# Kernel optimization log

Measured on AMD Instinct MI355X. Metric: run time of the kernel, lower is better.

## Reference

```python
import jax, jax.numpy as jnp
import numpy as np

N_NODES = 100000
N_EDGES = 3200000
N_GRAPHS = 4096
IN_DIM = 128
HID = 64
EPS = 1e-5


def setup_inputs() -> dict:
    key = jax.random.key(0)
    ks = jax.random.split(key, 16)
    x = jax.random.normal(ks[0], (N_NODES, IN_DIM), dtype=jnp.float32)
    edge_index = jax.random.randint(ks[1], (2, N_EDGES), 0, N_NODES, dtype=jnp.int32)
    batch = jnp.sort(jax.random.randint(ks[2], (N_NODES,), 0, N_GRAPHS, dtype=jnp.int32))

    def lin(k, fan_in, fan_out):
        s = 1.0 / np.sqrt(fan_in)
        kw, kb = jax.random.split(k)
        W = jax.random.uniform(kw, (fan_in, fan_out), minval=-s, maxval=s, dtype=jnp.float32)
        b = jax.random.uniform(kb, (fan_out,), minval=-s, maxval=s, dtype=jnp.float32)
        return W, b

    Wc0, bc0 = lin(ks[3], IN_DIM, HID)
    Wc1, bc1 = lin(ks[4], HID, HID)
    Wc2, bc2 = lin(ks[5], HID, HID)
    W1, b1 = lin(ks[6], HID, HID)
    W2, b2 = lin(ks[7], HID, 1)
    ones = jnp.ones((HID,), jnp.float32)
    zeros = jnp.zeros((HID,), jnp.float32)
    return {
        'x': x, 'edge_index': edge_index, 'batch': batch,
        'Wc0': Wc0, 'bc0': bc0, 'g0': ones, 'be0': zeros,
        'Wc1': Wc1, 'bc1': bc1, 'g1': ones, 'be1': zeros,
        'Wc2': Wc2, 'bc2': bc2, 'g2': ones, 'be2': zeros,
        'W1': W1, 'b1': b1, 'gf': ones, 'bf': zeros,
        'W2': W2, 'b2': b2,
    }


def _gcn_norm(edge_index):
    # Add self-loops, then symmetric normalization norm_e = d^-1/2[row] * d^-1/2[col]
    loops = jnp.arange(N_NODES, dtype=jnp.int32)
    row = jnp.concatenate([edge_index[0], loops])
    col = jnp.concatenate([edge_index[1], loops])
    deg = jax.ops.segment_sum(jnp.ones_like(col, jnp.float32), col, num_segments=N_NODES)
    dinv = jnp.where(deg > 0, jax.lax.rsqrt(deg), 0.0)
    norm = dinv[row] * dinv[col]
    return row, col, norm


def _gcn_conv(x, W, b, row, col, norm):
    h = x @ W                                   # [N, hid]
    msg = h[row] * norm[:, None]                # [E+N, hid] gather + scale
    out = jax.ops.segment_sum(msg, col, num_segments=N_NODES)  # scatter-add
    return out + b


def _bn(x, gamma, beta):
    mu = jnp.mean(x, axis=0)
    var = jnp.var(x, axis=0)
    return (x - mu) * jax.lax.rsqrt(var + EPS) * gamma + beta


def reference(x, edge_index, batch, Wc0, bc0, g0, be0, Wc1, bc1, g1, be1,
              Wc2, bc2, g2, be2, W1, b1, gf, bf, W2, b2):
    row, col, norm = _gcn_norm(edge_index)
    h = x
    for W, b, g, be in ((Wc0, bc0, g0, be0), (Wc1, bc1, g1, be1), (Wc2, bc2, g2, be2)):
        h = jax.nn.relu(_bn(_gcn_conv(h, W, b, row, col, norm), g, be))
    # global mean pool over graphs
    sums = jax.ops.segment_sum(h, batch, num_segments=N_GRAPHS)
    cnts = jax.ops.segment_sum(jnp.ones((N_NODES,), jnp.float32), batch, num_segments=N_GRAPHS)
    pooled = sums / jnp.maximum(cnts, 1.0)[:, None]  # [G, hid]
    z = jax.nn.relu(_bn(pooled @ W1 + b1, gf, bf))
    # dropout is identity at inference
    out = z @ W2 + b2
    return out.squeeze(-1)
```

## Files before the change

### kernel.cpp

```cpp
#include <hip/hip_runtime.h>
#include <hip/hip_bf16.h>

#define NN 100000
#define NE 3200000
#define NG 4096
#define NB 256
#define NBK 782

typedef unsigned short ushort_t;
typedef short short8 __attribute__((ext_vector_type(8)));
typedef float floatx4 __attribute__((ext_vector_type(4)));

__device__ __forceinline__ float bf2f(unsigned short u){
  union{unsigned int i; float f;} x; x.i = ((unsigned)u)<<16; return x.f;
}
__device__ __forceinline__ ushort_t f2bf(float f){
  union{float f; unsigned int i;} x; x.f = f;
  unsigned int r = x.i + 0x7fff + ((x.i >> 16) & 1);
  return (ushort_t)(r >> 16);
}


__global__ __launch_bounds__(512) void k_hist(const int* __restrict__ ei, int* __restrict__ histT){
  __shared__ int lh[NBK];
  int b = blockIdx.x, t = threadIdx.x;
  for (int k=t; k<NBK; k+=512) lh[k]=0;
  __syncthreads();
  int e0 = b*(NE/NB);
  for (int e=e0+t; e<e0+(NE/NB); e+=512) atomicAdd(&lh[ei[NE+e]>>7], 1);
  __syncthreads();
  for (int k=t; k<NBK; k+=512) histT[(size_t)k*NB+b] = lh[k];
}

__global__ __launch_bounds__(256) void k_scanA(int* __restrict__ histT, int* __restrict__ total){
  int wv = blockIdx.x*4 + (threadIdx.x>>6);
  int lane = threadIdx.x & 63;
  if (wv >= NBK) return;
  int* row = histT + (size_t)wv*NB;
  int carry = 0;
  #pragma unroll
  for (int ch=0; ch<NB/64; ++ch){
    int a = row[ch*64+lane];
    int inc = a;
    for (int off=1; off<64; off<<=1){
      int x = __shfl_up(inc, off, 64);
      if (lane >= off) inc += x;
    }
    row[ch*64+lane] = carry + inc - a;
    carry += __shfl(inc, 63, 64);
  }
  if (lane==0) total[wv] = carry;
}

__global__ void k_scanB(const int* __restrict__ total, int* __restrict__ base){
  __shared__ int lds[1024];
  int t = threadIdx.x;
  int v = (t < NBK)? total[t] : 0;
  lds[t] = v; __syncthreads();
  for (int off=1; off<1024; off<<=1){
    int x = (t>=off)? lds[t-off] : 0;
    __syncthreads();
    lds[t] += x;
    __syncthreads();
  }
  if (t < NBK)      base[t]   = lds[t]-v;
  if (t == NBK-1)   base[NBK] = lds[t];
}

__global__ __launch_bounds__(512) void k_pairs(const int* __restrict__ ei,
    const int* __restrict__ histT, const int* __restrict__ base,
    int* __restrict__ pairs){
  __shared__ int cur[NBK];
  int b = blockIdx.x, t = threadIdx.x;
  for (int k=t; k<NBK; k+=512) cur[k] = base[k] + histT[(size_t)k*NB + b];
  __syncthreads();
  int e0 = b*(NE/NB);
  for (int e=e0+t; e<e0+(NE/NB); e+=512){
    int src = ei[e], dst = ei[NE+e];
    int p = atomicAdd(&cur[dst>>7], 1);
    pairs[p] = (src << 7) | (dst & 127);
  }
}

__global__ __launch_bounds__(256) void k_fine(const int* __restrict__ pairs,
    const int* __restrict__ base, int* __restrict__ csr,
    int* __restrict__ colptr, float* __restrict__ dinv){
  __shared__ int cnt[128], off[128];
  int k = blockIdx.x, t = threadIdx.x;
  if (t < 128) cnt[t] = 0;
  __syncthreads();
  int s = base[k], e = base[k+1];
  for (int i=s+t; i<e; i+=256) atomicAdd(&cnt[pairs[i] & 127], 1);
  __syncthreads();
  int v = (t<128)? cnt[t] : 0;
  if (t<128) off[t] = v;
  __syncthreads();
  for (int o=1; o<128; o<<=1){
    int x = (t>=o && t<128)? off[t-o] : 0;
    __syncthreads();
    if (t<128) off[t] += x;
    __syncthreads();
  }
  int node0 = k*128;
  if (t < 128 && node0+t < NN){
    colptr[node0+t] = s + off[t] - v;
    dinv[node0+t]   = rsqrtf((float)cnt[t] + 1.0f);
  }
  if (k == NBK-1 && t == 0) colptr[NN] = NE;
  __syncthreads();
  if (t < 128) cnt[t] = off[t] - v;
  __syncthreads();
  for (int i=s+t; i<e; i+=256){
    int u = pairs[i];
    int p = s + atomicAdd(&cnt[u & 127], 1);
    csr[p] = u >> 7;
  }
}


__global__ __launch_bounds__(256) void k_gemm0m(const float* __restrict__ x,
    const float* __restrict__ W, const float* __restrict__ dinv,
    ushort_t* __restrict__ hs){
  __shared__ __attribute__((aligned(16))) ushort_t Wt[64*136];
  int t = threadIdx.x;
  for (int i=t; i<128*64; i+=256){
    int k = i>>6, n = i&63;
    Wt[n*136 + k] = f2bf(W[i]);
  }
  __syncthreads();
  int lane = t & 63, wv = t >> 6;
  int n0 = lane & 15, quad = lane >> 4;
  int r0 = blockIdx.x*64 + wv*16;
  int row = r0 + n0;
  int rowc = (row < NN)? row : NN-1;
  const float* xr = x + (size_t)rowc*128 + quad*8;
  floatx4 acc[4] = {{0,0,0,0},{0,0,0,0},{0,0,0,0},{0,0,0,0}};
  #pragma unroll
  for (int ks=0; ks<4; ++ks){
    float4 a01 = *(const float4*)(xr + ks*32);
    float4 a23 = *(const float4*)(xr + ks*32 + 4);
    short8 af;
    af[0]=(short)f2bf(a01.x); af[1]=(short)f2bf(a01.y);
    af[2]=(short)f2bf(a01.z); af[3]=(short)f2bf(a01.w);
    af[4]=(short)f2bf(a23.x); af[5]=(short)f2bf(a23.y);
    af[6]=(short)f2bf(a23.z); af[7]=(short)f2bf(a23.w);
    #pragma unroll
    for (int tl=0; tl<4; ++tl){
      short8 bf = *(const short8*)(&Wt[(tl*16+n0)*136 + ks*32 + quad*8]);
      acc[tl] = __builtin_amdgcn_mfma_f32_16x16x32_bf16(af, bf, acc[tl], 0, 0, 0);
    }
  }
  #pragma unroll
  for (int reg=0; reg<4; ++reg){
    int rr = r0 + quad*4 + reg;
    if (rr < NN){
      float dv = dinv[rr];
      #pragma unroll
      for (int tl=0; tl<4; ++tl)
        hs[(size_t)rr*64 + tl*16 + n0] = f2bf(acc[tl][reg]*dv);
    }
  }
}


__global__ __launch_bounds__(256) void k_gemmSm(const float* __restrict__ h,
    const float* __restrict__ W, const float* __restrict__ coeff,
    const float* __restrict__ dinv, ushort_t* __restrict__ hs){
  __shared__ __attribute__((aligned(16))) ushort_t Wt[64*72];
  int t = threadIdx.x;
  for (int i=t; i<64*64; i+=256){
    int k = i>>6, n = i&63;
    Wt[n*72 + k] = f2bf(W[i]);
  }
  __syncthreads();
  int lane = t & 63, wv = t >> 6;
  int n0 = lane & 15, quad = lane >> 4;
  int r0 = blockIdx.x*64 + wv*16;
  int row = r0 + n0;
  int rowc = (row < NN)? row : NN-1;
  const float* hr = h + (size_t)rowc*64 + quad*8;
  floatx4 acc[4] = {{0,0,0,0},{0,0,0,0},{0,0,0,0},{0,0,0,0}};
  #pragma unroll
  for (int ks=0; ks<2; ++ks){
    float4 a01 = *(const float4*)(hr + ks*32);
    float4 a23 = *(const float4*)(hr + ks*32 + 4);
    const float* cA = coeff + ks*32 + quad*8;
    float4 ca0 = *(const float4*)(cA),      ca1 = *(const float4*)(cA+4);
    float4 cb0 = *(const float4*)(cA+64),   cb1 = *(const float4*)(cA+68);
    short8 af;
    af[0]=(short)f2bf(fmaxf(fmaf(a01.x,ca0.x,cb0.x),0.f));
    af[1]=(short)f2bf(fmaxf(fmaf(a01.y,ca0.y,cb0.y),0.f));
    af[2]=(short)f2bf(fmaxf(fmaf(a01.z,ca0.z,cb0.z),0.f));
    af[3]=(short)f2bf(fmaxf(fmaf(a01.w,ca0.w,cb0.w),0.f));
    af[4]=(short)f2bf(fmaxf(fmaf(a23.x,ca1.x,cb1.x),0.f));
    af[5]=(short)f2bf(fmaxf(fmaf(a23.y,ca1.y,cb1.y),0.f));
    af[6]=(short)f2bf(fmaxf(fmaf(a23.z,ca1.z,cb1.z),0.f));
    af[7]=(short)f2bf(fmaxf(fmaf(a23.w,ca1.w,cb1.w),0.f));
    #pragma unroll
    for (int tl=0; tl<4; ++tl){
      short8 bf = *(const short8*)(&Wt[(tl*16+n0)*72 + ks*32 + quad*8]);
      acc[tl] = __builtin_amdgcn_mfma_f32_16x16x32_bf16(af, bf, acc[tl], 0, 0, 0);
    }
  }
  #pragma unroll
  for (int reg=0; reg<4; ++reg){
    int rr = r0 + quad*4 + reg;
    if (rr < NN){
      float dv = dinv[rr];
      #pragma unroll
      for (int tl=0; tl<4; ++tl)
        hs[(size_t)rr*64 + tl*16 + n0] = f2bf(acc[tl][reg]*dv);
    }
  }
}


__global__ __launch_bounds__(256) void k_aggregate(const ushort_t* __restrict__ hs,
    const int* __restrict__ colptr, const int* __restrict__ csr,
    const float* __restrict__ dinv, const float* __restrict__ bias,
    float* __restrict__ out, float* __restrict__ stats){
  int t = threadIdx.x; int c = t & 63;
  int wv = blockIdx.x*4 + (t>>6);
  float bc = bias[c];
  float s1 = 0.f, s2 = 0.f;
  for (int v = wv; v < NN; v += 8192){
    int vv = __builtin_amdgcn_readfirstlane(v);
    int e0 = colptr[vv], e1 = colptr[vv+1];
    float acc = bf2f(hs[(size_t)vv*64 + c]);
    int e = e0;
    for (; e+8 <= e1; e += 8){
      int i0=csr[e],   i1=csr[e+1], i2=csr[e+2], i3=csr[e+3];
      int i4=csr[e+4], i5=csr[e+5], i6=csr[e+6], i7=csr[e+7];
      float f0=bf2f(hs[(size_t)i0*64+c]), f1=bf2f(hs[(size_t)i1*64+c]);
      float f2=bf2f(hs[(size_t)i2*64+c]), f3=bf2f(hs[(size_t)i3*64+c]);
      float f4=bf2f(hs[(size_t)i4*64+c]), f5=bf2f(hs[(size_t)i5*64+c]);
      float f6=bf2f(hs[(size_t)i6*64+c]), f7=bf2f(hs[(size_t)i7*64+c]);
      acc += ((f0+f1)+(f2+f3)) + ((f4+f5)+(f6+f7));
    }
    for (; e+4 <= e1; e += 4){
      int i0=csr[e], i1=csr[e+1], i2=csr[e+2], i3=csr[e+3];
      float f0=bf2f(hs[(size_t)i0*64+c]), f1=bf2f(hs[(size_t)i1*64+c]);
      float f2=bf2f(hs[(size_t)i2*64+c]), f3=bf2f(hs[(size_t)i3*64+c]);
      acc += (f0+f1)+(f2+f3);
    }
    for (; e<e1; ++e) acc += bf2f(hs[(size_t)csr[e]*64+c]);
    float o = acc*dinv[vv] + bc;
    out[(size_t)vv*64+c] = o;
    s1 += o; s2 += o*o;
  }
  __shared__ float l1[256], l2[256];
  l1[t]=s1; l2[t]=s2; __syncthreads();
  if (t < 64){
    float a1 = l1[t]+l1[t+64]+l1[t+128]+l1[t+192];
    float a2 = l2[t]+l2[t+64]+l2[t+128]+l2[t+192];
    float* rep = stats + (size_t)(blockIdx.x & 31)*128;
    atomicAdd(&rep[t],    a1);
    atomicAdd(&rep[64+t], a2);
  }
}


__global__ void k_bncoeff(const float* __restrict__ stats, const float* __restrict__ g,
                          const float* __restrict__ be, float cnt, float* __restrict__ coeff){
  int c = threadIdx.x;
  float s1=0.f, s2=0.f;
  for (int r=0;r<32;++r){ s1 += stats[r*128+c]; s2 += stats[r*128+64+c]; }
  float mu  = s1/cnt;
  float var = s2/cnt - mu*mu;
  float a   = g[c]*rsqrtf(var + 1e-5f);
  coeff[c]    = a;
  coeff[64+c] = be[c] - mu*a;
}


__global__ __launch_bounds__(256) void k_gbounds(const int* __restrict__ batch, int* __restrict__ gstart){
  int g = blockIdx.x*256 + threadIdx.x;
  int lo=0, hi=NN;
  while (lo<hi){ int mid=(lo+hi)>>1; if (batch[mid]<g) lo=mid+1; else hi=mid; }
  gstart[g]=lo;
  if (g==0) gstart[NG]=NN;
}

__global__ __launch_bounds__(256) void k_pool(const float* __restrict__ h, const int* __restrict__ gstart,
                                              const float* __restrict__ cf, float* __restrict__ pooled){
  int t=threadIdx.x; int c=t&63;
  int g = __builtin_amdgcn_readfirstlane((int)(blockIdx.x*4 + (t>>6)));
  int s = gstart[g], e = gstart[g+1];
  float a = cf[c], d = cf[64+c];
  float acc=0.f;
  for (int v=s; v<e; ++v) acc += fmaxf(fmaf(h[(size_t)v*64+c], a, d), 0.f);
  float inv = 1.0f / fmaxf((float)(e-s), 1.0f);
  pooled[(size_t)g*64+c] = acc*inv;
}

__global__ __launch_bounds__(256) void k_tkern(float* __restrict__ pooled, const float* __restrict__ W1,
                                               const float* __restrict__ b1, float* __restrict__ stats){
  int t=threadIdx.x; int c=t&63;
  int g = __builtin_amdgcn_readfirstlane((int)(blockIdx.x*4 + (t>>6)));
  const float* p = pooled + (size_t)g*64;
  float acc = b1[c];
  #pragma unroll 4
  for (int k=0;k<64;++k) acc = fmaf(p[k], W1[k*64+c], acc);
  pooled[(size_t)g*64+c] = acc;
  float* rep = stats + (size_t)(blockIdx.x & 31)*128;
  atomicAdd(&rep[c],    acc);
  atomicAdd(&rep[64+c], acc*acc);
}

__global__ __launch_bounds__(256) void k_final(const float* __restrict__ tbuf, const float* __restrict__ gcf,
                                               const float* __restrict__ W2, const float* __restrict__ b2,
                                               float* __restrict__ out){
  int t=threadIdx.x; int c=t&63;
  int g = blockIdx.x*4 + (t>>6);
  float tv = tbuf[(size_t)g*64+c];
  float z  = fmaxf(fmaf(tv, gcf[c], gcf[64+c]), 0.f);
  float p  = z * W2[c];
  #pragma unroll
  for (int o=32;o>0;o>>=1) p += __shfl_xor(p, o, 64);
  if (c==0) out[g] = p + b2[0];
}


extern "C" void kernel_launch(void* const* d_in, const int* in_sizes, int n_in,
                              void* d_out, int out_size, void* d_ws, size_t ws_size,
                              hipStream_t stream) {
  const float* x    = (const float*)d_in[0];
  const int*   ei   = (const int*)d_in[1];
  const int*   batch= (const int*)d_in[2];
  const float* Wc0=(const float*)d_in[3],  *bc0=(const float*)d_in[4];
  const float* g0 =(const float*)d_in[5],  *be0=(const float*)d_in[6];
  const float* Wc1=(const float*)d_in[7],  *bc1=(const float*)d_in[8];
  const float* g1 =(const float*)d_in[9],  *be1=(const float*)d_in[10];
  const float* Wc2=(const float*)d_in[11], *bc2=(const float*)d_in[12];
  const float* g2 =(const float*)d_in[13], *be2=(const float*)d_in[14];
  const float* W1 =(const float*)d_in[15], *b1 =(const float*)d_in[16];
  const float* gf =(const float*)d_in[17], *bf_=(const float*)d_in[18];
  const float* W2 =(const float*)d_in[19], *b2 =(const float*)d_in[20];
  float* out = (float*)d_out;

  char* w = (char*)d_ws;
  float*    stats  = (float*)   (w + 0);
  int*      total  = (int*)     (w + 65536);
  int*      base   = (int*)     (w + 68736);
  int*      colptr = (int*)     (w + 71936);
  float*    dinv   = (float*)   (w + 471952);
  int*      gstart = (int*)     (w + 871952);
  float*    coeff  = (float*)   (w + 888352);
  float*    gcoeff = (float*)   (w + 888864);
  float*    pooled = (float*)   (w + 889376);
  int*      csr    = (int*)     (w + 1937968);
  ushort_t* bufA   = (ushort_t*)(w + 14737968);
  float*    bufB   = (float*)   (w + 27537968);
  int*      histT  = csr;
  int*      pairs  = (int*)bufB;

  hipMemsetAsync(stats, 0, 65536, stream);

  k_hist <<<NB,  512,  0, stream>>>(ei, histT);
  k_scanA<<<196, 256,  0, stream>>>(histT, total);
  k_scanB<<<1,   1024, 0, stream>>>(total, base);
  k_pairs<<<NB,  512,  0, stream>>>(ei, histT, base, pairs);
  k_fine <<<NBK, 256,  0, stream>>>(pairs, base, csr, colptr, dinv);

  k_gemm0m<<<1563, 256, 0, stream>>>(x, Wc0, dinv, bufA);
  k_aggregate<<<2048, 256, 0, stream>>>(bufA, colptr, csr, dinv, bc0, bufB, stats + 0*4096);
  k_bncoeff<<<1, 64, 0, stream>>>(stats + 0*4096, g0, be0, (float)NN, coeff);
  k_gemmSm<<<1563, 256, 0, stream>>>(bufB, Wc1, coeff, dinv, bufA);
  k_aggregate<<<2048, 256, 0, stream>>>(bufA, colptr, csr, dinv, bc1, bufB, stats + 1*4096);
  k_bncoeff<<<1, 64, 0, stream>>>(stats + 1*4096, g1, be1, (float)NN, coeff);
  k_gemmSm<<<1563, 256, 0, stream>>>(bufB, Wc2, coeff, dinv, bufA);
  k_aggregate<<<2048, 256, 0, stream>>>(bufA, colptr, csr, dinv, bc2, bufB, stats + 2*4096);
  k_bncoeff<<<1, 64, 0, stream>>>(stats + 2*4096, g2, be2, (float)NN, coeff);

  k_gbounds<<<NG/256, 256, 0, stream>>>(batch, gstart);
  k_pool   <<<NG/4,   256, 0, stream>>>(bufB, gstart, coeff, pooled);
  k_tkern  <<<NG/4,   256, 0, stream>>>(pooled, W1, b1, stats + 3*4096);
  k_bncoeff<<<1, 64, 0, stream>>>(stats + 3*4096, gf, bf_, (float)NG, gcoeff);
  k_final  <<<NG/4,   256, 0, stream>>>(pooled, gcoeff, W2, b2, out);
}
```

Before: 556.8 us.

## Fold BN coefficient kernels into last-block epilogues and cut launches

Each BN-coefficient kernel is removed. Instead, the last block to finish aggregate or tkern (chosen with an atomic ticket) computes the coefficients. The memset is folded into k_hist, the gbounds kernel is inlined into k_pool as binary searches, and histogram blocks and fine-sort threads are doubled. The goal is to cut kernel launch count and the serial tiny-kernel gaps, at the cost of fence and atomic overhead plus redundant binary searches in the pool kernel.

```diff
diff --git a/kernel.cpp b/kernel.cpp
--- a/kernel.cpp
+++ b/kernel.cpp
@@ -4,7 +4,7 @@
 #define NN 100000
 #define NE 3200000
 #define NG 4096
-#define NB 256
+#define NB 512
 #define NBK 782
 
 typedef unsigned short ushort_t;
@@ -21,9 +21,12 @@
 }
 
 
-__global__ __launch_bounds__(512) void k_hist(const int* __restrict__ ei, int* __restrict__ histT){
+__global__ __launch_bounds__(512) void k_hist(const int* __restrict__ ei, int* __restrict__ histT,
+                                              float4* __restrict__ zbase){
   __shared__ int lh[NBK];
   int b = blockIdx.x, t = threadIdx.x;
+  int gtid = b*512 + t;
+  if (gtid < 4098) zbase[gtid] = make_float4(0.f,0.f,0.f,0.f);
   for (int k=t; k<NBK; k+=512) lh[k]=0;
   __syncthreads();
   int e0 = b*(NE/NB);
@@ -82,7 +85,7 @@
   }
 }
 
-__global__ __launch_bounds__(256) void k_fine(const int* __restrict__ pairs,
+__global__ __launch_bounds__(512) void k_fine(const int* __restrict__ pairs,
     const int* __restrict__ base, int* __restrict__ csr,
     int* __restrict__ colptr, float* __restrict__ dinv){
   __shared__ int cnt[128], off[128];
@@ -90,7 +93,7 @@
   if (t < 128) cnt[t] = 0;
   __syncthreads();
   int s = base[k], e = base[k+1];
-  for (int i=s+t; i<e; i+=256) atomicAdd(&cnt[pairs[i] & 127], 1);
+  for (int i=s+t; i<e; i+=512) atomicAdd(&cnt[pairs[i] & 127], 1);
   __syncthreads();
   int v = (t<128)? cnt[t] : 0;
   if (t<128) off[t] = v;
@@ -110,7 +113,7 @@
   __syncthreads();
   if (t < 128) cnt[t] = off[t] - v;
   __syncthreads();
-  for (int i=s+t; i<e; i+=256){
+  for (int i=s+t; i<e; i+=512){
     int u = pairs[i];
     int p = s + atomicAdd(&cnt[u & 127], 1);
     csr[p] = u >> 7;
@@ -218,7 +221,9 @@
 __global__ __launch_bounds__(256) void k_aggregate(const ushort_t* __restrict__ hs,
     const int* __restrict__ colptr, const int* __restrict__ csr,
     const float* __restrict__ dinv, const float* __restrict__ bias,
-    float* __restrict__ out, float* __restrict__ stats){
+    float* __restrict__ out, float* __restrict__ stats,
+    const float* __restrict__ g, const float* __restrict__ be,
+    float* __restrict__ coeff, int* __restrict__ ticket){
   int t = threadIdx.x; int c = t & 63;
   int wv = blockIdx.x*4 + (t>>6);
   float bc = bias[c];
@@ -249,6 +254,7 @@
     s1 += o; s2 += o*o;
   }
   __shared__ float l1[256], l2[256];
+  __shared__ int amLast;
   l1[t]=s1; l2[t]=s2; __syncthreads();
   if (t < 64){
     float a1 = l1[t]+l1[t+64]+l1[t+128]+l1[t+192];
@@ -257,35 +263,34 @@
     atomicAdd(&rep[t],    a1);
     atomicAdd(&rep[64+t], a2);
   }
-}
-
-
-__global__ void k_bncoeff(const float* __restrict__ stats, const float* __restrict__ g,
-                          const float* __restrict__ be, float cnt, float* __restrict__ coeff){
-  int c = threadIdx.x;
-  float s1=0.f, s2=0.f;
-  for (int r=0;r<32;++r){ s1 += stats[r*128+c]; s2 += stats[r*128+64+c]; }
-  float mu  = s1/cnt;
-  float var = s2/cnt - mu*mu;
-  float a   = g[c]*rsqrtf(var + 1e-5f);
-  coeff[c]    = a;
-  coeff[64+c] = be[c] - mu*a;
-}
-
-
-__global__ __launch_bounds__(256) void k_gbounds(const int* __restrict__ batch, int* __restrict__ gstart){
-  int g = blockIdx.x*256 + threadIdx.x;
-  int lo=0, hi=NN;
-  while (lo<hi){ int mid=(lo+hi)>>1; if (batch[mid]<g) lo=mid+1; else hi=mid; }
-  gstart[g]=lo;
-  if (g==0) gstart[NG]=NN;
-}
-
-__global__ __launch_bounds__(256) void k_pool(const float* __restrict__ h, const int* __restrict__ gstart,
+  __threadfence();
+  if (t == 0) amLast = (atomicAdd(ticket, 1) == 2047);
+  __syncthreads();
+  if (amLast && t < 64){
+    float u1=0.f, u2=0.f;
+    for (int r=0;r<32;++r){
+      u1 += __hip_atomic_load(&stats[r*128+t],    __ATOMIC_RELAXED, __HIP_MEMORY_SCOPE_AGENT);
+      u2 += __hip_atomic_load(&stats[r*128+64+t], __ATOMIC_RELAXED, __HIP_MEMORY_SCOPE_AGENT);
+    }
+    float mu  = u1/(float)NN;
+    float var = u2/(float)NN - mu*mu;
+    float a   = g[t]*rsqrtf(var + 1e-5f);
+    coeff[t]    = a;
+    coeff[64+t] = be[t] - mu*a;
+  }
+}
+
+
+__global__ __launch_bounds__(256) void k_pool(const float* __restrict__ h, const int* __restrict__ batch,
                                               const float* __restrict__ cf, float* __restrict__ pooled){
   int t=threadIdx.x; int c=t&63;
   int g = __builtin_amdgcn_readfirstlane((int)(blockIdx.x*4 + (t>>6)));
-  int s = gstart[g], e = gstart[g+1];
+  int lo=0, hi=NN;
+  while (lo<hi){ int mid=(lo+hi)>>1; if (batch[mid]<g) lo=mid+1; else hi=mid; }
+  int s = lo;
+  hi = NN;
+  while (lo<hi){ int mid=(lo+hi)>>1; if (batch[mid]<g+1) lo=mid+1; else hi=mid; }
+  int e = lo;
   float a = cf[c], d = cf[64+c];
   float acc=0.f;
   for (int v=s; v<e; ++v) acc += fmaxf(fmaf(h[(size_t)v*64+c], a, d), 0.f);
@@ -293,8 +298,11 @@
   pooled[(size_t)g*64+c] = acc*inv;
 }
 
+
 __global__ __launch_bounds__(256) void k_tkern(float* __restrict__ pooled, const float* __restrict__ W1,
-                                               const float* __restrict__ b1, float* __restrict__ stats){
+                                               const float* __restrict__ b1, float* __restrict__ stats,
+                                               const float* __restrict__ gf, const float* __restrict__ bf_,
+                                               float* __restrict__ gcoeff, int* __restrict__ ticket){
   int t=threadIdx.x; int c=t&63;
   int g = __builtin_amdgcn_readfirstlane((int)(blockIdx.x*4 + (t>>6)));
   const float* p = pooled + (size_t)g*64;
@@ -305,6 +313,22 @@
   float* rep = stats + (size_t)(blockIdx.x & 31)*128;
   atomicAdd(&rep[c],    acc);
   atomicAdd(&rep[64+c], acc*acc);
+  __shared__ int amLast;
+  __threadfence();
+  if (t == 0) amLast = (atomicAdd(ticket, 1) == 1023);
+  __syncthreads();
+  if (amLast && t < 64){
+    float u1=0.f, u2=0.f;
+    for (int r=0;r<32;++r){
+      u1 += __hip_atomic_load(&stats[r*128+t],    __ATOMIC_RELAXED, __HIP_MEMORY_SCOPE_AGENT);
+      u2 += __hip_atomic_load(&stats[r*128+64+t], __ATOMIC_RELAXED, __HIP_MEMORY_SCOPE_AGENT);
+    }
+    float mu  = u1/(float)NG;
+    float var = u2/(float)NG - mu*mu;
+    float a   = gf[t]*rsqrtf(var + 1e-5f);
+    gcoeff[t]    = a;
+    gcoeff[64+t] = bf_[t] - mu*a;
+  }
 }
 
 __global__ __launch_bounds__(256) void k_final(const float* __restrict__ tbuf, const float* __restrict__ gcf,
@@ -340,41 +364,37 @@
 
   char* w = (char*)d_ws;
   float*    stats  = (float*)   (w + 0);
-  int*      total  = (int*)     (w + 65536);
-  int*      base   = (int*)     (w + 68736);
-  int*      colptr = (int*)     (w + 71936);
-  float*    dinv   = (float*)   (w + 471952);
-  int*      gstart = (int*)     (w + 871952);
-  float*    coeff  = (float*)   (w + 888352);
-  float*    gcoeff = (float*)   (w + 888864);
-  float*    pooled = (float*)   (w + 889376);
-  int*      csr    = (int*)     (w + 1937968);
-  ushort_t* bufA   = (ushort_t*)(w + 14737968);
-  float*    bufB   = (float*)   (w + 27537968);
+  int*      ticket = (int*)     (w + 65536);
+  int*      total  = (int*)     (w + 65568);
+  int*      base   = (int*)     (w + 68704);
+  int*      colptr = (int*)     (w + 71840);
+  float*    dinv   = (float*)   (w + 471856);
+  float*    coeff  = (float*)   (w + 871856);
+  float*    gcoeff = (float*)   (w + 872368);
+  float*    pooled = (float*)   (w + 872880);
+  int*      csr    = (int*)     (w + 1921456);
+  ushort_t* bufA   = (ushort_t*)(w + 14721456);
+  float*    bufB   = (float*)   (w + 27521456);
   int*      histT  = csr;
   int*      pairs  = (int*)bufB;
 
-  hipMemsetAsync(stats, 0, 65536, stream);
-
-  k_hist <<<NB,  512,  0, stream>>>(ei, histT);
+  k_hist <<<NB,  512,  0, stream>>>(ei, histT, (float4*)w);
   k_scanA<<<196, 256,  0, stream>>>(histT, total);
   k_scanB<<<1,   1024, 0, stream>>>(total, base);
   k_pairs<<<NB,  512,  0, stream>>>(ei, histT, base, pairs);
-  k_fine <<<NBK, 256,  0, stream>>>(pairs, base, csr, colptr, dinv);
+  k_fine <<<NBK, 512,  0, stream>>>(pairs, base, csr, colptr, dinv);
 
   k_gemm0m<<<1563, 256, 0, stream>>>(x, Wc0, dinv, bufA);
-  k_aggregate<<<2048, 256, 0, stream>>>(bufA, colptr, csr, dinv, bc0, bufB, stats + 0*4096);
-  k_bncoeff<<<1, 64, 0, stream>>>(stats + 0*4096, g0, be0, (float)NN, coeff);
+  k_aggregate<<<2048, 256, 0, stream>>>(bufA, colptr, csr, dinv, bc0, bufB, stats + 0*4096,
+                                        g0, be0, coeff, ticket + 0);
   k_gemmSm<<<1563, 256, 0, stream>>>(bufB, Wc1, coeff, dinv, bufA);
-  k_aggregate<<<2048, 256, 0, stream>>>(bufA, colptr, csr, dinv, bc1, bufB, stats + 1*4096);
-  k_bncoeff<<<1, 64, 0, stream>>>(stats + 1*4096, g1, be1, (float)NN, coeff);
+  k_aggregate<<<2048, 256, 0, stream>>>(bufA, colptr, csr, dinv, bc1, bufB, stats + 1*4096,
+                                        g1, be1, coeff, ticket + 1);
   k_gemmSm<<<1563, 256, 0, stream>>>(bufB, Wc2, coeff, dinv, bufA);
-  k_aggregate<<<2048, 256, 0, stream>>>(bufA, colptr, csr, dinv, bc2, bufB, stats + 2*4096);
-  k_bncoeff<<<1, 64, 0, stream>>>(stats + 2*4096, g2, be2, (float)NN, coeff);
-
-  k_gbounds<<<NG/256, 256, 0, stream>>>(batch, gstart);
-  k_pool   <<<NG/4,   256, 0, stream>>>(bufB, gstart, coeff, pooled);
-  k_tkern  <<<NG/4,   256, 0, stream>>>(pooled, W1, b1, stats + 3*4096);
-  k_bncoeff<<<1, 64, 0, stream>>>(stats + 3*4096, gf, bf_, (float)NG, gcoeff);
-  k_final  <<<NG/4,   256, 0, stream>>>(pooled, gcoeff, W2, b2, out);
-}
+  k_aggregate<<<2048, 256, 0, stream>>>(bufA, colptr, csr, dinv, bc2, bufB, stats + 2*4096,
+                                        g2, be2, coeff, ticket + 2);
+
+  k_pool <<<NG/4, 256, 0, stream>>>(bufB, batch, coeff, pooled);
+  k_tkern<<<NG/4, 256, 0, stream>>>(pooled, W1, b1, stats + 3*4096, gf, bf_, gcoeff, ticket + 3);
+  k_final<<<NG/4, 256, 0, stream>>>(pooled, gcoeff, W2, b2, out);
+}
```

Result: slower. 1.295 ms (+132.6%).
